# Kernel tuning notes

Measured on AMD Instinct MI355X. Metric: run time of the kernel, lower is better.

Reference implementation:

```python
import jax, jax.numpy as jnp
import numpy as np

B, T, V, H = 256, 512, 64, 256
IN = 2 * V + 1  # values + masks + delta_t = 129


def setup_inputs() -> dict:
    key = jax.random.key(0)
    ks = jax.random.split(key, 8)
    # sorted positive times with some entries zeroed (ragged padding -> t_exist False)
    t = jnp.sort(jax.random.uniform(ks[0], (B, T)), axis=1)
    keep = jax.random.uniform(ks[1], (B, T)) < 0.9
    times_in = jnp.where(keep, t, 0.0).astype(jnp.float32)
    data_in = jax.random.normal(ks[2], (B, T, V), dtype=jnp.float32)
    mask_in = (jax.random.uniform(ks[3], (B, T, V)) < 0.8).astype(jnp.float32)
    s = 1.0 / np.sqrt(H).astype(np.float32)
    W_ih = jax.random.uniform(ks[4], (3 * H, IN), minval=-s, maxval=s, dtype=jnp.float32)
    W_hh = jax.random.uniform(ks[5], (3 * H, H), minval=-s, maxval=s, dtype=jnp.float32)
    b_ih = jax.random.uniform(ks[6], (3 * H,), minval=-s, maxval=s, dtype=jnp.float32)
    b_hh = jax.random.uniform(ks[7], (3 * H,), minval=-s, maxval=s, dtype=jnp.float32)
    return {"times_in": times_in, "data_in": data_in, "mask_in": mask_in,
            "W_ih": W_ih, "W_hh": W_hh, "b_ih": b_ih, "b_hh": b_hh}


def reference(times_in, data_in, mask_in, W_ih, W_hh, b_ih, b_hh):
    b = times_in.shape[0]
    # delta_ts: times[:,1:] - times[:,:-1], padded with zero at the end
    delta = jnp.concatenate(
        [times_in[:, 1:] - times_in[:, :-1],
         jnp.zeros((b, 1), times_in.dtype)], axis=1)  # [B,T]
    # input_series = cat(values, masks, delta_t) -> [B,T,2V+1]
    x = jnp.concatenate([data_in, mask_in, delta[..., None]], axis=-1)
    t_exist = times_in > 0  # [B,T]
    h0 = jnp.zeros((b, W_hh.shape[1]), x.dtype)

    xs = (jnp.swapaxes(x, 0, 1), jnp.swapaxes(t_exist, 0, 1))  # time-major

    def step(h, inp):
        xt, m = inp  # xt: [B,IN], m: [B]
        gx = xt @ W_ih.T + b_ih  # [B,3H]
        gh = h @ W_hh.T + b_hh   # [B,3H]
        xr, xz, xn = jnp.split(gx, 3, axis=-1)
        hr, hz, hn = jnp.split(gh, 3, axis=-1)
        r = jax.nn.sigmoid(xr + hr)
        z = jax.nn.sigmoid(xz + hz)
        n = jnp.tanh(xn + r * hn)
        h_new = (1.0 - z) * n + z * h
        h = jnp.where(m[:, None], h_new, h)  # masked state carry
        return h, None

    h_final, _ = jax.lax.scan(step, h0, xs)
    return h_final
```

## Files before the change

### kernel.cpp

```cpp
#include <hip/hip_runtime.h>

#define Bn 256
#define Tn 512
#define Vn 64
#define Hn 256
#define INn 129
#define Cc 8
#define NCH (Tn / Cc)
#define WU 68
#define WSZ (768 * WU)
#define GX_OFF (262144)
#define GX_BYTES ((size_t)Bn * Tn * 768 * 2)
#define AST 168
#define CST 264

typedef __fp16 half2_t __attribute__((ext_vector_type(2)));
typedef __fp16 half8_t __attribute__((ext_vector_type(8)));
typedef float f32x4 __attribute__((ext_vector_type(4)));

static __device__ __forceinline__ unsigned int cvt2(float a, float b) {
  return __builtin_bit_cast(unsigned int, __builtin_amdgcn_cvt_pkrtz(a, b));
}

static __device__ __forceinline__ float dot2(unsigned int w, unsigned int x, float acc) {
#if __has_builtin(__builtin_amdgcn_fdot2)
  return __builtin_amdgcn_fdot2(__builtin_bit_cast(half2_t, w),
                                __builtin_bit_cast(half2_t, x), acc, false);
#else
  half2_t a = __builtin_bit_cast(half2_t, w);
  half2_t b = __builtin_bit_cast(half2_t, x);
  return acc + (float)a.x * (float)b.x + (float)a.y * (float)b.y;
#endif
}

static __device__ __forceinline__ float pair_sum(float v) {
#if __has_builtin(__builtin_amdgcn_update_dpp)
  int x = __builtin_amdgcn_update_dpp(0, __builtin_bit_cast(int, v), 0xB1, 0xF, 0xF, true);
  return v + __builtin_bit_cast(float, x);
#else
  int j = __builtin_amdgcn_ds_swizzle(__builtin_bit_cast(int, v), 0x041F);
  return v + __builtin_bit_cast(float, j);
#endif
}

static __device__ __forceinline__ float fast_exp2(float x) {
#if __has_builtin(__builtin_amdgcn_exp2f)
  return __builtin_amdgcn_exp2f(x);
#else
  return exp2f(x);
#endif
}
static __device__ __forceinline__ float fast_rcp(float x) {
#if __has_builtin(__builtin_amdgcn_rcpf)
  return __builtin_amdgcn_rcpf(x);
#else
  return 1.f / x;
#endif
}
static __device__ __forceinline__ float sigmoid_f(float x) {
  return fast_rcp(1.f + fast_exp2(-1.44269504f * x));
}
static __device__ __forceinline__ float tanh_f(float x) {
  return 1.f - 2.f * fast_rcp(1.f + fast_exp2(2.88539008f * x));
}

__global__ void convert_wih(const float* __restrict__ W_ih, unsigned int* __restrict__ w16) {
  int idx = blockIdx.x * 256 + threadIdx.x;
  if (idx >= WSZ) return;
  int j = idx / WU, c = idx - j * WU;
  int col = 2 * c;
  float f0 = (col < INn) ? W_ih[(size_t)j * INn + col] : 0.f;
  float f1 = (col + 1 < INn) ? W_ih[(size_t)j * INn + col + 1] : 0.f;
  w16[idx] = cvt2(f0, f1);
}

__global__ __launch_bounds__(256, 4)
void gx_gemm(const float* __restrict__ times_in, const float* __restrict__ data_in,
             const float* __restrict__ mask_in, const unsigned int* __restrict__ w16,
             const float* __restrict__ b_ih, __fp16* __restrict__ gx) {
  __shared__ __align__(16) char raw[64 * CST * 2];
  __fp16* xa = (__fp16*)raw;
  __fp16* ct = (__fp16*)raw;

  const int tid = threadIdx.x;
  const int bt = blockIdx.x;
  const int b = bt >> 3, tc = bt & 7;
  const int t0 = tc * 64;
  const int n0 = blockIdx.y * 256;

  {
    int r = tid >> 2, s = tid & 3;
    const float* src = (s < 2)
        ? data_in + ((size_t)b * Tn + t0 + r) * Vn + s * 32
        : mask_in + ((size_t)b * Tn + t0 + r) * Vn + (s - 2) * 32;
    unsigned int* dst = (unsigned int*)(xa + r * AST) + s * 16;
#pragma unroll
    for (int i = 0; i < 8; ++i) {
      float4 v = ((const float4*)src)[i];
      dst[2 * i] = cvt2(v.x, v.y);
      dst[2 * i + 1] = cvt2(v.z, v.w);
    }
  }
  if (tid < 64) {
    int g = t0 + tid;
    float tcur = times_in[(size_t)b * Tn + g];
    float d = (g < Tn - 1) ? times_in[(size_t)b * Tn + g + 1] - tcur : 0.f;
    unsigned int* p = (unsigned int*)(xa + tid * AST + 128);
    p[0] = cvt2(d, 0.f);
#pragma unroll
    for (int i = 1; i < 20; ++i) p[i] = 0u;
  }
  __syncthreads();

  const int w = tid >> 6, lane = tid & 63;
  const int m = lane & 15, q = lane >> 4;
  const int nw = n0 + w * 64;

  f32x4 acc[4][4];
#pragma unroll
  for (int i = 0; i < 4; ++i)
#pragma unroll
    for (int j = 0; j < 4; ++j) acc[i][j] = f32x4{0.f, 0.f, 0.f, 0.f};

#pragma unroll
  for (int kt = 0; kt < 5; ++kt) {
    const int k0 = kt * 32 + q * 8;
    half8_t bf[4], af[4];
#pragma unroll
    for (int nt = 0; nt < 4; ++nt) {
      int n = nw + nt * 16 + m;
      uint4 bv = *(const uint4*)(w16 + (size_t)n * WU + (k0 >> 1));
      bf[nt] = __builtin_bit_cast(half8_t, bv);
    }
#pragma unroll
    for (int mt = 0; mt < 4; ++mt) {
      uint4 av = *(const uint4*)(xa + (mt * 16 + m) * AST + k0);
      af[mt] = __builtin_bit_cast(half8_t, av);
    }
#pragma unroll
    for (int mt = 0; mt < 4; ++mt)
#pragma unroll
      for (int nt = 0; nt < 4; ++nt)
        acc[mt][nt] = __builtin_amdgcn_mfma_f32_16x16x32_f16(af[mt], bf[nt], acc[mt][nt], 0, 0, 0);
  }

  float bias[4];
#pragma unroll
  for (int nt = 0; nt < 4; ++nt) bias[nt] = b_ih[nw + nt * 16 + m];

  __syncthreads();
#pragma unroll
  for (int mt = 0; mt < 4; ++mt)
#pragma unroll
    for (int nt = 0; nt < 4; ++nt)
#pragma unroll
      for (int r = 0; r < 4; ++r)
        ct[(mt * 16 + q * 4 + r) * CST + w * 64 + nt * 16 + m] =
            (__fp16)(acc[mt][nt][r] + bias[nt]);
  __syncthreads();

  {
    const int tt = tid >> 2, qq = tid & 3;
    const uint4* src = (const uint4*)(ct + tt * CST) + qq * 8;
    uint4* dst = (uint4*)(gx + ((size_t)b * Tn + t0 + tt) * 768 + n0) + qq * 8;
#pragma unroll
    for (int i = 0; i < 8; ++i) dst[i] = src[i];
  }
}

__global__ __launch_bounds__(512, 1)
void gru_scan2(const float* __restrict__ times_in, const float* __restrict__ W_hh,
               const float* __restrict__ b_hh, const __fp16* __restrict__ gx,
               float* __restrict__ out) {
  __shared__ __align__(16) __fp16 h_buf[2 * Hn];
  __shared__ __align__(16) float t_lds[Tn];

  const int tid = threadIdx.x;
  const int b = blockIdx.x;
  const int jg = tid >> 1;
  const int ks = tid & 1;

  t_lds[tid] = times_in[(size_t)b * Tn + tid];

  unsigned int whr[64], whz[64], whn[64];
  {
    const float* w0 = W_hh + (size_t)jg * Hn + ks * 128;
    const float* w1 = W_hh + (size_t)(jg + 256) * Hn + ks * 128;
    const float* w2 = W_hh + (size_t)(jg + 512) * Hn + ks * 128;
#pragma unroll
    for (int c = 0; c < 64; ++c) {
      whr[c] = cvt2(w0[2 * c], w0[2 * c + 1]);
      whz[c] = cvt2(w1[2 * c], w1[2 * c + 1]);
      whn[c] = cvt2(w2[2 * c], w2[2 * c + 1]);
    }
  }
  const float brh = b_hh[jg];
  const float bzh = b_hh[jg + 256];
  const float bhn = b_hh[jg + 512];

  h_buf[tid] = (__fp16)0.f;
  __syncthreads();

  const __fp16* gxb = gx + (size_t)b * Tn * 768;
  float hcur = 0.f;

  float gr = (float)gxb[jg], gz = (float)gxb[256 + jg], gn = (float)gxb[512 + jg];
  float mt = t_lds[0];

#pragma unroll 1
  for (int t = 0; t < Tn; ++t) {
    __fp16 pr = (__fp16)0.f, pz = (__fp16)0.f, pn = (__fp16)0.f;
    float mtn = 0.f;
    if (t + 1 < Tn) {
      const __fp16* p = gxb + (size_t)(t + 1) * 768;
      pr = p[jg]; pz = p[256 + jg]; pn = p[512 + jg];
      mtn = t_lds[t + 1];
    }

    const int cur = t & 1;
    const uint4* hb = (const uint4*)(h_buf + cur * Hn) + ks * 16;

    float sr = 0.f, sz = 0.f, shn = 0.f;
    uint4 p0 = hb[0], p1 = hb[1];
#pragma unroll
    for (int cc = 0; cc < 8; ++cc) {
      uint4 q0 = p0, q1 = p1;
      if (cc < 7) { q0 = hb[2 * cc + 2]; q1 = hb[2 * cc + 3]; }
      const int cb = cc * 8;
      sr = dot2(whr[cb + 0], p0.x, sr);
      sz = dot2(whz[cb + 0], p0.x, sz);
      shn = dot2(whn[cb + 0], p0.x, shn);
      sr = dot2(whr[cb + 1], p0.y, sr);
      sz = dot2(whz[cb + 1], p0.y, sz);
      shn = dot2(whn[cb + 1], p0.y, shn);
      sr = dot2(whr[cb + 2], p0.z, sr);
      sz = dot2(whz[cb + 2], p0.z, sz);
      shn = dot2(whn[cb + 2], p0.z, shn);
      sr = dot2(whr[cb + 3], p0.w, sr);
      sz = dot2(whz[cb + 3], p0.w, sz);
      shn = dot2(whn[cb + 3], p0.w, shn);
      sr = dot2(whr[cb + 4], p1.x, sr);
      sz = dot2(whz[cb + 4], p1.x, sz);
      shn = dot2(whn[cb + 4], p1.x, shn);
      sr = dot2(whr[cb + 5], p1.y, sr);
      sz = dot2(whz[cb + 5], p1.y, sz);
      shn = dot2(whn[cb + 5], p1.y, shn);
      sr = dot2(whr[cb + 6], p1.z, sr);
      sz = dot2(whz[cb + 6], p1.z, sz);
      shn = dot2(whn[cb + 6], p1.z, shn);
      sr = dot2(whr[cb + 7], p1.w, sr);
      sz = dot2(whz[cb + 7], p1.w, sz);
      shn = dot2(whn[cb + 7], p1.w, shn);
      p0 = q0; p1 = q1;
    }

    sr = pair_sum(sr);
    sz = pair_sum(sz);
    shn = pair_sum(shn);

    float r = sigmoid_f(gr + sr + brh);
    float z = sigmoid_f(gz + sz + bzh);
    float n = tanh_f(gn + r * (shn + bhn));
    float hN = (1.f - z) * n + z * hcur;
    hcur = (mt > 0.f) ? hN : hcur;

    if (ks == 0) h_buf[(cur ^ 1) * Hn + jg] = (__fp16)hcur;
    __syncthreads();

    gr = (float)pr; gz = (float)pz; gn = (float)pn; mt = mtn;
  }

  if (ks == 0) out[(size_t)b * Hn + jg] = hcur;
}

template <bool USE_WS>
static __device__ __forceinline__ void phaseA_pass(int col, const unsigned int* __restrict__ w16,
                                                   const float* __restrict__ W_ih,
                                                   const unsigned int* x_lds, float* a) {
  const uint4* wp = (const uint4*)(w16) + (size_t)col * (WU / 4);
  const float* wf = W_ih + (size_t)col * INn;
#pragma unroll 2
  for (int kp = 0; kp < 8; ++kp) {
    uint4 wa, wb;
    if constexpr (USE_WS) {
      wa = wp[2 * kp];
      wb = wp[2 * kp + 1];
    } else {
      const float* f = wf + 16 * kp;
      wa.x = cvt2(f[0], f[1]);   wa.y = cvt2(f[2], f[3]);
      wa.z = cvt2(f[4], f[5]);   wa.w = cvt2(f[6], f[7]);
      wb.x = cvt2(f[8], f[9]);   wb.y = cvt2(f[10], f[11]);
      wb.z = cvt2(f[12], f[13]); wb.w = cvt2(f[14], f[15]);
    }
#pragma unroll
    for (int t = 0; t < Cc; ++t) {
      const uint4* xp = (const uint4*)&x_lds[t * WU + kp * 8];
      uint4 xa = xp[0], xb = xp[1];
      a[t] = dot2(wa.x, xa.x, a[t]);
      a[t] = dot2(wa.y, xa.y, a[t]);
      a[t] = dot2(wa.z, xa.z, a[t]);
      a[t] = dot2(wa.w, xa.w, a[t]);
      a[t] = dot2(wb.x, xb.x, a[t]);
      a[t] = dot2(wb.y, xb.y, a[t]);
      a[t] = dot2(wb.z, xb.z, a[t]);
      a[t] = dot2(wb.w, xb.w, a[t]);
    }
  }
  uint4 wt;
  if constexpr (USE_WS) {
    wt = wp[16];
  } else {
    wt.x = cvt2(wf[128], 0.f); wt.y = 0u; wt.z = 0u; wt.w = 0u;
  }
#pragma unroll
  for (int t = 0; t < Cc; ++t) {
    uint4 xt = *(const uint4*)&x_lds[t * WU + 64];
    a[t] = dot2(wt.x, xt.x, a[t]);
    a[t] = dot2(wt.y, xt.y, a[t]);
  }
}

template <bool USE_WS>
__global__ __launch_bounds__(512, 2)
void gru_scan_fb(const float* __restrict__ times_in, const float* __restrict__ data_in,
                 const float* __restrict__ mask_in, const unsigned int* __restrict__ w16,
                 const float* __restrict__ W_ih, const float* __restrict__ W_hh,
                 const float* __restrict__ b_ih, const float* __restrict__ b_hh,
                 float* __restrict__ out) {
  __shared__ __align__(16) float gx_lds[Cc * 768];
  __shared__ __align__(16) unsigned int x_lds[Cc * WU];
  __shared__ __align__(16) __fp16 h_buf[2 * Hn];
  __shared__ __align__(16) float t_lds[Tn];

  const int tid = threadIdx.x;
  const int b = blockIdx.x;
  const int jg = tid >> 1;
  const int ks = tid & 1;

  t_lds[tid] = times_in[(size_t)b * Tn + tid];

  unsigned int whr[64], whz[64], whn[64];
  {
    const float* w0 = W_hh + (size_t)jg * Hn + ks * 128;
    const float* w1 = W_hh + (size_t)(jg + 256) * Hn + ks * 128;
    const float* w2 = W_hh + (size_t)(jg + 512) * Hn + ks * 128;
#pragma unroll
    for (int c = 0; c < 64; ++c) {
      whr[c] = cvt2(w0[2 * c], w0[2 * c + 1]);
      whz[c] = cvt2(w1[2 * c], w1[2 * c + 1]);
      whn[c] = cvt2(w2[2 * c], w2[2 * c + 1]);
    }
  }
  const float brh = b_hh[jg];
  const float bzh = b_hh[jg + 256];
  const float bhn = b_hh[jg + 512];
  const float bi1 = b_ih[tid];
  const float bi2 = (tid < 256) ? b_ih[512 + tid] : 0.f;

  h_buf[tid] = (__fp16)0.f;
  __syncthreads();

  float hcur = 0.f;
  int cur = 0;
#pragma unroll 1
  for (int ch = 0; ch < NCH; ++ch) {
    const int t0 = ch * Cc;
    {
      int t = tid >> 6;
      int c = tid & 63;
      const float* src = (c < 32)
          ? data_in + ((size_t)b * Tn + t0 + t) * Vn + 2 * c
          : mask_in + ((size_t)b * Tn + t0 + t) * Vn + 2 * (c - 32);
      float2 v = *(const float2*)src;
      x_lds[t * WU + c] = cvt2(v.x, v.y);
      if (tid < Cc) {
        int g = t0 + tid;
        float d = (g < Tn - 1) ? (t_lds[g + 1] - t_lds[g]) : 0.f;
        uint4 tl;
        tl.x = cvt2(d, 0.f); tl.y = 0u; tl.z = 0u; tl.w = 0u;
        *(uint4*)&x_lds[tid * WU + 64] = tl;
      }
    }
    __syncthreads();
    {
      float a[Cc];
#pragma unroll
      for (int t = 0; t < Cc; ++t) a[t] = bi1;
      phaseA_pass<USE_WS>(tid, w16, W_ih, x_lds, a);
#pragma unroll
      for (int t = 0; t < Cc; ++t) gx_lds[t * 768 + tid] = a[t];
      if (tid < 256) {
#pragma unroll
        for (int t = 0; t < Cc; ++t) a[t] = bi2;
        phaseA_pass<USE_WS>(512 + tid, w16, W_ih, x_lds, a);
#pragma unroll
        for (int t = 0; t < Cc; ++t) gx_lds[t * 768 + 512 + tid] = a[t];
      }
    }
    __syncthreads();
    for (int tt = 0; tt < Cc; ++tt) {
      float sr = 0.f, sz = 0.f, shn = 0.f;
      const uint4* hb = (const uint4*)(h_buf + cur * Hn + ks * 128);
#pragma unroll
      for (int c = 0; c < 16; ++c) {
        uint4 hv = hb[c];
        sr = dot2(whr[4 * c + 0], hv.x, sr);
        sz = dot2(whz[4 * c + 0], hv.x, sz);
        shn = dot2(whn[4 * c + 0], hv.x, shn);
        sr = dot2(whr[4 * c + 1], hv.y, sr);
        sz = dot2(whz[4 * c + 1], hv.y, sz);
        shn = dot2(whn[4 * c + 1], hv.y, shn);
        sr = dot2(whr[4 * c + 2], hv.z, sr);
        sz = dot2(whz[4 * c + 2], hv.z, sz);
        shn = dot2(whn[4 * c + 2], hv.z, shn);
        sr = dot2(whr[4 * c + 3], hv.w, sr);
        sz = dot2(whz[4 * c + 3], hv.w, sz);
        shn = dot2(whn[4 * c + 3], hv.w, shn);
      }
      float gxr = gx_lds[tt * 768 + jg];
      float gxz = gx_lds[tt * 768 + 256 + jg];
      float gxn = gx_lds[tt * 768 + 512 + jg];
      sr = pair_sum(sr);
      sz = pair_sum(sz);
      shn = pair_sum(shn);
      float r = sigmoid_f(gxr + sr + brh);
      float z = sigmoid_f(gxz + sz + bzh);
      float n = tanh_f(gxn + r * (shn + bhn));
      float hN = (1.f - z) * n + z * hcur;
      hcur = (t_lds[t0 + tt] > 0.f) ? hN : hcur;
      if (ks == 0) h_buf[(cur ^ 1) * Hn + jg] = (__fp16)hcur;
      __syncthreads();
      cur ^= 1;
    }
  }
  if (ks == 0) out[(size_t)b * Hn + jg] = hcur;
}

extern "C" void kernel_launch(void* const* d_in, const int* in_sizes, int n_in,
                              void* d_out, int out_size, void* d_ws, size_t ws_size,
                              hipStream_t stream) {
  const float* times_in = (const float*)d_in[0];
  const float* data_in = (const float*)d_in[1];
  const float* mask_in = (const float*)d_in[2];
  const float* W_ih = (const float*)d_in[3];
  const float* W_hh = (const float*)d_in[4];
  const float* b_ih = (const float*)d_in[5];
  const float* b_hh = (const float*)d_in[6];
  float* out = (float*)d_out;

  unsigned int* w16 = (unsigned int*)d_ws;
  __fp16* gx = (__fp16*)((char*)d_ws + GX_OFF);

  if (ws_size >= GX_OFF + GX_BYTES) {
    hipLaunchKernelGGL(convert_wih, dim3((WSZ + 255) / 256), dim3(256), 0, stream, W_ih, w16);
    hipLaunchKernelGGL(gx_gemm, dim3(2048, 3), dim3(256), 0, stream,
                       times_in, data_in, mask_in, w16, b_ih, gx);
    hipLaunchKernelGGL(gru_scan2, dim3(Bn), dim3(512), 0, stream,
                       times_in, W_hh, b_hh, gx, out);
  } else if (ws_size >= (size_t)WSZ * 4) {
    hipLaunchKernelGGL(convert_wih, dim3((WSZ + 255) / 256), dim3(256), 0, stream, W_ih, w16);
    hipLaunchKernelGGL((gru_scan_fb<true>), dim3(Bn), dim3(512), 0, stream,
                       times_in, data_in, mask_in, w16, W_ih, W_hh, b_ih, b_hh, out);
  } else {
    hipLaunchKernelGGL((gru_scan_fb<false>), dim3(Bn), dim3(512), 0, stream,
                       times_in, data_in, mask_in, (const unsigned int*)nullptr, W_ih, W_hh,
                       b_ih, b_hh, out);
  }
}
```

Before: 778.0 us.

## Split GRU recurrent dot product across four lanes per hidden unit

The scan kernel now uses 1024 threads per block, with four lanes sharing each hidden unit instead of two. Each lane holds a quarter of the W_hh row in registers (96 instead of 192), and a two-step DPP quad reduction replaces the pair sum. This halves the serial dot-product length per time step, which is the latency on the recurrence's critical path. In exchange it adds reduction steps, doubles barrier participants, and doubles the redundant gx loads and gate math per hidden unit. The prefetch branch for the next step is also replaced with an index clamp.

Result: slower. 858.5 us (+10.3%).

```diff
diff --git a/kernel.cpp b/kernel.cpp
--- a/kernel.cpp
+++ b/kernel.cpp
@@ -43,6 +43,22 @@
 #endif
 }
 
+static __device__ __forceinline__ float quad_sum(float v) {
+#if __has_builtin(__builtin_amdgcn_update_dpp)
+  int x = __builtin_amdgcn_update_dpp(0, __builtin_bit_cast(int, v), 0xB1, 0xF, 0xF, true);
+  v += __builtin_bit_cast(float, x);
+  int y = __builtin_amdgcn_update_dpp(0, __builtin_bit_cast(int, v), 0x4E, 0xF, 0xF, true);
+  v += __builtin_bit_cast(float, y);
+  return v;
+#else
+  int j = __builtin_amdgcn_ds_swizzle(__builtin_bit_cast(int, v), 0x041F);
+  v += __builtin_bit_cast(float, j);
+  j = __builtin_amdgcn_ds_swizzle(__builtin_bit_cast(int, v), 0x081F);
+  v += __builtin_bit_cast(float, j);
+  return v;
+#endif
+}
+
 static __device__ __forceinline__ float fast_exp2(float x) {
 #if __has_builtin(__builtin_amdgcn_exp2f)
   return __builtin_amdgcn_exp2f(x);
@@ -168,8 +184,18 @@
   }
 }
 
-__global__ __launch_bounds__(512, 1)
-void gru_scan2(const float* __restrict__ times_in, const float* __restrict__ W_hh,
+#define DOT4(hv, base)                                                                     \
+  sr = dot2(whr[(base) + 0], hv.x, sr); sz = dot2(whz[(base) + 0], hv.x, sz);              \
+  shn = dot2(whn[(base) + 0], hv.x, shn);                                                  \
+  sr = dot2(whr[(base) + 1], hv.y, sr); sz = dot2(whz[(base) + 1], hv.y, sz);              \
+  shn = dot2(whn[(base) + 1], hv.y, shn);                                                  \
+  sr = dot2(whr[(base) + 2], hv.z, sr); sz = dot2(whz[(base) + 2], hv.z, sz);              \
+  shn = dot2(whn[(base) + 2], hv.z, shn);                                                  \
+  sr = dot2(whr[(base) + 3], hv.w, sr); sz = dot2(whz[(base) + 3], hv.w, sz);              \
+  shn = dot2(whn[(base) + 3], hv.w, shn);
+
+__global__ __launch_bounds__(1024, 1)
+void gru_scan4(const float* __restrict__ times_in, const float* __restrict__ W_hh,
                const float* __restrict__ b_hh, const __fp16* __restrict__ gx,
                float* __restrict__ out) {
   __shared__ __align__(16) __fp16 h_buf[2 * Hn];
@@ -177,18 +203,18 @@
 
   const int tid = threadIdx.x;
   const int b = blockIdx.x;
-  const int jg = tid >> 1;
-  const int ks = tid & 1;
-
-  t_lds[tid] = times_in[(size_t)b * Tn + tid];
-
-  unsigned int whr[64], whz[64], whn[64];
+  const int jg = tid >> 2;
+  const int ks = tid & 3;
+
+  if (tid < Tn) t_lds[tid] = times_in[(size_t)b * Tn + tid];
+
+  unsigned int whr[32], whz[32], whn[32];
   {
-    const float* w0 = W_hh + (size_t)jg * Hn + ks * 128;
-    const float* w1 = W_hh + (size_t)(jg + 256) * Hn + ks * 128;
-    const float* w2 = W_hh + (size_t)(jg + 512) * Hn + ks * 128;
-#pragma unroll
-    for (int c = 0; c < 64; ++c) {
+    const float* w0 = W_hh + (size_t)jg * Hn + ks * 64;
+    const float* w1 = W_hh + (size_t)(jg + 256) * Hn + ks * 64;
+    const float* w2 = W_hh + (size_t)(jg + 512) * Hn + ks * 64;
+#pragma unroll
+    for (int c = 0; c < 32; ++c) {
       whr[c] = cvt2(w0[2 * c], w0[2 * c + 1]);
       whz[c] = cvt2(w1[2 * c], w1[2 * c + 1]);
       whn[c] = cvt2(w2[2 * c], w2[2 * c + 1]);
@@ -198,7 +224,7 @@
   const float bzh = b_hh[jg + 256];
   const float bhn = b_hh[jg + 512];
 
-  h_buf[tid] = (__fp16)0.f;
+  if (tid < 2 * Hn) h_buf[tid] = (__fp16)0.f;
   __syncthreads();
 
   const __fp16* gxb = gx + (size_t)b * Tn * 768;
@@ -209,54 +235,27 @@
 
 #pragma unroll 1
   for (int t = 0; t < Tn; ++t) {
-    __fp16 pr = (__fp16)0.f, pz = (__fp16)0.f, pn = (__fp16)0.f;
-    float mtn = 0.f;
-    if (t + 1 < Tn) {
-      const __fp16* p = gxb + (size_t)(t + 1) * 768;
-      pr = p[jg]; pz = p[256 + jg]; pn = p[512 + jg];
-      mtn = t_lds[t + 1];
-    }
+    const int tn = (t + 1 < Tn) ? (t + 1) : (Tn - 1);
+    const __fp16* p = gxb + (size_t)tn * 768;
+    __fp16 pr = p[jg], pz = p[256 + jg], pn = p[512 + jg];
+    float mtn = t_lds[tn];
 
     const int cur = t & 1;
-    const uint4* hb = (const uint4*)(h_buf + cur * Hn) + ks * 16;
+    const uint4* hb = (const uint4*)(h_buf + cur * Hn) + ks * 8;
 
     float sr = 0.f, sz = 0.f, shn = 0.f;
-    uint4 p0 = hb[0], p1 = hb[1];
-#pragma unroll
-    for (int cc = 0; cc < 8; ++cc) {
-      uint4 q0 = p0, q1 = p1;
-      if (cc < 7) { q0 = hb[2 * cc + 2]; q1 = hb[2 * cc + 3]; }
-      const int cb = cc * 8;
-      sr = dot2(whr[cb + 0], p0.x, sr);
-      sz = dot2(whz[cb + 0], p0.x, sz);
-      shn = dot2(whn[cb + 0], p0.x, shn);
-      sr = dot2(whr[cb + 1], p0.y, sr);
-      sz = dot2(whz[cb + 1], p0.y, sz);
-      shn = dot2(whn[cb + 1], p0.y, shn);
-      sr = dot2(whr[cb + 2], p0.z, sr);
-      sz = dot2(whz[cb + 2], p0.z, sz);
-      shn = dot2(whn[cb + 2], p0.z, shn);
-      sr = dot2(whr[cb + 3], p0.w, sr);
-      sz = dot2(whz[cb + 3], p0.w, sz);
-      shn = dot2(whn[cb + 3], p0.w, shn);
-      sr = dot2(whr[cb + 4], p1.x, sr);
-      sz = dot2(whz[cb + 4], p1.x, sz);
-      shn = dot2(whn[cb + 4], p1.x, shn);
-      sr = dot2(whr[cb + 5], p1.y, sr);
-      sz = dot2(whz[cb + 5], p1.y, sz);
-      shn = dot2(whn[cb + 5], p1.y, shn);
-      sr = dot2(whr[cb + 6], p1.z, sr);
-      sz = dot2(whz[cb + 6], p1.z, sz);
-      shn = dot2(whn[cb + 6], p1.z, shn);
-      sr = dot2(whr[cb + 7], p1.w, sr);
-      sz = dot2(whz[cb + 7], p1.w, sz);
-      shn = dot2(whn[cb + 7], p1.w, shn);
-      p0 = q0; p1 = q1;
-    }
-
-    sr = pair_sum(sr);
-    sz = pair_sum(sz);
-    shn = pair_sum(shn);
+    {
+      uint4 h0 = hb[0], h1 = hb[1], h2 = hb[2], h3 = hb[3];
+      DOT4(h0, 0) DOT4(h1, 4) DOT4(h2, 8) DOT4(h3, 12)
+    }
+    {
+      uint4 h4 = hb[4], h5 = hb[5], h6 = hb[6], h7 = hb[7];
+      DOT4(h4, 16) DOT4(h5, 20) DOT4(h6, 24) DOT4(h7, 28)
+    }
+
+    sr = quad_sum(sr);
+    sz = quad_sum(sz);
+    shn = quad_sum(shn);
 
     float r = sigmoid_f(gr + sr + brh);
     float z = sigmoid_f(gz + sz + bzh);
@@ -455,7 +454,7 @@
     hipLaunchKernelGGL(convert_wih, dim3((WSZ + 255) / 256), dim3(256), 0, stream, W_ih, w16);
     hipLaunchKernelGGL(gx_gemm, dim3(2048, 3), dim3(256), 0, stream,
                        times_in, data_in, mask_in, w16, b_ih, gx);
-    hipLaunchKernelGGL(gru_scan2, dim3(Bn), dim3(512), 0, stream,
+    hipLaunchKernelGGL(gru_scan4, dim3(Bn), dim3(1024), 0, stream,
                        times_in, W_hh, b_hh, gx, out);
   } else if (ws_size >= (size_t)WSZ * 4) {
     hipLaunchKernelGGL(convert_wih, dim3((WSZ + 255) / 256), dim3(256), 0, stream, W_ih, w16);
```
